# Performance work log

Hardware: AMD Instinct MI355X
Metric: run time of the kernel (lower is better)

The kernel has to match this reference:

```python
import jax, jax.numpy as jnp
import numpy as np

B, H, D = 16, 16, 128
BLOCK = 16
BLOCKS_PER_SEQ = 128
MAX_S = BLOCK * BLOCKS_PER_SEQ  # 2048
NUM_BLOCKS = B * BLOCKS_PER_SEQ  # 2048


def _rotate_half(x):
    d = x.shape[-1] // 2
    return jnp.concatenate([-x[..., d:], x[..., :d]], axis=-1)


def setup_inputs() -> dict:
    key = jax.random.key(0)
    ks = jax.random.split(key, 8)
    Q = jax.random.normal(ks[0], (B, H, D), dtype=jnp.float32)
    K = jax.random.normal(ks[1], (B, H, D), dtype=jnp.float32)
    V = jax.random.normal(ks[2], (B, H, D), dtype=jnp.float32)
    Kcache = jax.random.normal(ks[3], (NUM_BLOCKS, BLOCK, H, D), dtype=jnp.float32)
    Vcache = jax.random.normal(ks[4], (NUM_BLOCKS, BLOCK, H, D), dtype=jnp.float32)
    # RoPE tables [MAX_S, 1, D] (llama convention: half-dim freqs duplicated)
    inv_freq = 1.0 / (10000.0 ** (np.arange(0, D, 2, dtype=np.float32) / D))
    t = np.arange(MAX_S, dtype=np.float32)
    ang = np.einsum('t,f->tf', t, inv_freq)  # [MAX_S, D/2]
    emb = np.concatenate([ang, ang], axis=-1)  # [MAX_S, D]
    cos = jnp.asarray(np.cos(emb))[:, None, :]
    sin = jnp.asarray(np.sin(emb))[:, None, :]
    mask = jnp.zeros((B, MAX_S), dtype=jnp.float32)
    input_length = jnp.ones((B,), dtype=jnp.int32)
    cache_length = jax.random.randint(ks[5], (B,), 1024, MAX_S - 1).astype(jnp.int32)
    # block table: sequence b owns blocks [b*128, (b+1)*128)
    fetch_slots = (jnp.arange(B, dtype=jnp.int32)[:, None] * BLOCKS_PER_SEQ
                   + jnp.arange(BLOCKS_PER_SEQ, dtype=jnp.int32)[None, :])
    # write slot for the new token at position cache_length[b]
    blk = fetch_slots[jnp.arange(B), cache_length // BLOCK]
    save_slots = (blk * BLOCK + cache_length % BLOCK).astype(jnp.int32)
    return {"Q": Q, "K": K, "V": V, "Kcache": Kcache, "Vcache": Vcache,
            "cos": cos, "sin": sin, "mask": mask,
            "input_length": input_length, "cache_length": cache_length,
            "save_slots": save_slots, "fetch_slots": fetch_slots, "max_s": MAX_S}


def reference(Q, K, V, Kcache, Vcache, cos, sin, mask,
              input_length, cache_length, save_slots, fetch_slots, max_s):
    b, h, d = Q.shape
    block = Kcache.shape[1]
    scale = 1.0 / jnp.sqrt(jnp.asarray(d, Q.dtype))
    # RoPE on the new token at position cache_length[b]
    c = cos[cache_length]  # [B,1,D]
    s = sin[cache_length]
    Qr = Q * c + _rotate_half(Q) * s
    Kr = K * c + _rotate_half(K) * s
    # write new K/V into the paged caches at save_slots (flat slot ids)
    Kf = Kcache.reshape(-1, h, d).at[save_slots].set(Kr)
    Vf = Vcache.reshape(-1, h, d).at[save_slots].set(V)
    # gather per-sequence KV via block table -> flat slot ids [B, S]
    slot_ids = (fetch_slots[:, :, None] * block
                + jnp.arange(block, dtype=fetch_slots.dtype)).reshape(b, -1)
    Kg = Kf[slot_ids]  # [B,S,H,D]
    Vg = Vf[slot_ids]
    S = slot_ids.shape[1]
    scores = jnp.einsum('bhd,bshd->bhs', Qr, Kg) * scale + mask[:, None, :]
    valid = jnp.arange(S)[None, :] <= cache_length[:, None]  # [B,S]
    scores = jnp.where(valid[:, None, :], scores, jnp.finfo(scores.dtype).min)
    attn = jax.nn.softmax(scores, axis=-1)
    out = jnp.einsum('bhs,bshd->bhd', attn, Vg)
    return out
```

## Files before the change

kernel.cpp:

```cpp
#include <hip/hip_runtime.h>
#include <math.h>

#define PB_B      16
#define PB_H      16
#define PB_D      128
#define PB_BLOCK  16
#define PB_BPS    128
#define PB_MAXS   2048
#define PB_HD     (PB_H * PB_D)

#define NT        512
#define NSG       (NT / 32)

__global__ __launch_bounds__(NT) void paged_attn_decode(
    const float* __restrict__ Q,
    const float* __restrict__ Knew,
    const float* __restrict__ Vnew,
    const float* __restrict__ Kc,
    const float* __restrict__ Vc,
    const float* __restrict__ cosT,
    const float* __restrict__ sinT,
    const float* __restrict__ mask,
    const int*   __restrict__ cache_len,
    const int*   __restrict__ fetch_slots,
    float*       __restrict__ out)
{
    const int bh  = blockIdx.x;
    const int b   = bh >> 4;
    const int h   = bh & 15;
    const int tid = threadIdx.x;
    const int cl  = cache_len[b];
    const float scale = 0.08838834764831845f;

    __shared__ float sScore[PB_MAXS];
    __shared__ int   sSlots[PB_BPS];
    __shared__ float sQr[PB_D];
    __shared__ float sKr[PB_D];
    __shared__ float sRedM[NT / 64];
    __shared__ float sRedS[NT / 64];
    __shared__ float4 sAcc[NSG][32];

    if (tid < PB_BPS) sSlots[tid] = fetch_slots[b * PB_BPS + tid];

    if (tid < PB_D) {
        const float c = cosT[(size_t)cl * PB_D + tid];
        const float s = sinT[(size_t)cl * PB_D + tid];
        const float q = Q[(size_t)bh * PB_D + tid];
        const float k = Knew[(size_t)bh * PB_D + tid];
        const float qrot = (tid < 64) ? -Q[(size_t)bh * PB_D + tid + 64]
                                      :  Q[(size_t)bh * PB_D + tid - 64];
        const float krot = (tid < 64) ? -Knew[(size_t)bh * PB_D + tid + 64]
                                      :  Knew[(size_t)bh * PB_D + tid - 64];
        sQr[tid] = q * c + qrot * s;
        sKr[tid] = k * c + krot * s;
    }
    __syncthreads();

    const int dsub = tid & 31;
    const int ssub = tid >> 5;
    const float4 qv = ((const float4*)sQr)[dsub];
    const float* mrow = mask + (size_t)b * PB_MAXS;

    #pragma unroll 4
    for (int s = ssub; s < cl; s += NSG) {
        const int slot = sSlots[s >> 4] * PB_BLOCK + (s & 15);
        const float4 kv = ((const float4*)(Kc + (size_t)slot * PB_HD + (size_t)h * PB_D))[dsub];
        float dot = qv.x * kv.x + qv.y * kv.y + qv.z * kv.z + qv.w * kv.w;
        #pragma unroll
        for (int off = 16; off >= 1; off >>= 1) dot += __shfl_xor(dot, off);
        if (dsub == 0) sScore[s] = dot * scale + mrow[s];
    }
    if (tid < 32) {
        const float4 kv = ((const float4*)sKr)[dsub];
        float dot = qv.x * kv.x + qv.y * kv.y + qv.z * kv.z + qv.w * kv.w;
        #pragma unroll
        for (int off = 16; off >= 1; off >>= 1) dot += __shfl_xor(dot, off);
        if (dsub == 0) sScore[cl] = dot * scale + mrow[cl];
    }
    __syncthreads();

    float lm = -INFINITY;
    for (int s = tid; s <= cl; s += NT) lm = fmaxf(lm, sScore[s]);
    #pragma unroll
    for (int off = 32; off >= 1; off >>= 1) lm = fmaxf(lm, __shfl_xor(lm, off));
    if ((tid & 63) == 0) sRedM[tid >> 6] = lm;
    __syncthreads();
    float m = sRedM[0];
    #pragma unroll
    for (int w = 1; w < NT / 64; ++w) m = fmaxf(m, sRedM[w]);

    float ls = 0.0f;
    for (int s = tid; s <= cl; s += NT) {
        const float p = __expf(sScore[s] - m);
        sScore[s] = p;
        ls += p;
    }
    #pragma unroll
    for (int off = 32; off >= 1; off >>= 1) ls += __shfl_xor(ls, off);
    if ((tid & 63) == 0) sRedS[tid >> 6] = ls;
    __syncthreads();
    float sum = 0.0f;
    #pragma unroll
    for (int w = 0; w < NT / 64; ++w) sum += sRedS[w];

    float4 acc = make_float4(0.f, 0.f, 0.f, 0.f);
    #pragma unroll 4
    for (int s = ssub; s < cl; s += NSG) {
        const int slot = sSlots[s >> 4] * PB_BLOCK + (s & 15);
        const float4 vv = ((const float4*)(Vc + (size_t)slot * PB_HD + (size_t)h * PB_D))[dsub];
        const float p = sScore[s];
        acc.x += p * vv.x; acc.y += p * vv.y; acc.z += p * vv.z; acc.w += p * vv.w;
    }
    if (ssub == 0) {
        const float p = sScore[cl];
        const float4 vv = ((const float4*)(Vnew + (size_t)bh * PB_D))[dsub];
        acc.x += p * vv.x; acc.y += p * vv.y; acc.z += p * vv.z; acc.w += p * vv.w;
    }
    sAcc[ssub][dsub] = acc;
    __syncthreads();

    if (tid < 32) {
        float4 a = sAcc[0][tid];
        #pragma unroll
        for (int g = 1; g < NSG; ++g) {
            const float4 t = sAcc[g][tid];
            a.x += t.x; a.y += t.y; a.z += t.z; a.w += t.w;
        }
        const float inv = 1.0f / sum;
        a.x *= inv; a.y *= inv; a.z *= inv; a.w *= inv;
        ((float4*)(out + (size_t)bh * PB_D))[tid] = a;
    }
}

extern "C" void kernel_launch(void* const* d_in, const int* in_sizes, int n_in,
                              void* d_out, int out_size, void* d_ws, size_t ws_size,
                              hipStream_t stream) {
    const float* Q     = (const float*)d_in[0];
    const float* Knew  = (const float*)d_in[1];
    const float* Vnew  = (const float*)d_in[2];
    const float* Kc    = (const float*)d_in[3];
    const float* Vc    = (const float*)d_in[4];
    const float* cosT  = (const float*)d_in[5];
    const float* sinT  = (const float*)d_in[6];
    const float* mask  = (const float*)d_in[7];
    const int* cache_len   = (const int*)d_in[9];
    const int* fetch_slots = (const int*)d_in[11];
    float* out = (float*)d_out;

    paged_attn_decode<<<PB_B * PB_H, NT, 0, stream>>>(
        Q, Knew, Vnew, Kc, Vc, cosT, sinT, mask, cache_len, fetch_slots, out);
}
```

Before: 576.2 us.

## Split KV sequence across blocks with flash-decoding and a combine kernel

Splits each (batch, head) sequence into 8 chunks processed by separate 256-thread blocks, each producing a partial accumulator, max and sum in workspace; a second kernel merges them with log-sum-exp rescaling. The original grid of 256 blocks underfills the GPU, and the split is meant to raise parallelism and memory-level concurrency for this bandwidth-bound decode. It adds a second launch, a workspace round trip and redundant RoPE/slot loads per chunk.

New measurement: 499.6 us. 1.15x faster.

```diff
diff --git a/kernel.cpp b/kernel.cpp
--- a/kernel.cpp
+++ b/kernel.cpp
@@ -3,16 +3,19 @@
 
 #define PB_B      16
 #define PB_H      16
+#define PB_BH     (PB_B * PB_H)
 #define PB_D      128
 #define PB_BLOCK  16
 #define PB_BPS    128
 #define PB_MAXS   2048
 #define PB_HD     (PB_H * PB_D)
 
-#define NT        512
-#define NSG       (NT / 32)
-
-__global__ __launch_bounds__(NT) void paged_attn_decode(
+#define NSPLIT    8
+#define NT1       256
+#define NGRP      (NT1 / 32)
+#define MAXCHUNK  256
+
+__global__ __launch_bounds__(NT1) void pa_split(
     const float* __restrict__ Q,
     const float* __restrict__ Knew,
     const float* __restrict__ Vnew,
@@ -23,22 +26,39 @@
     const float* __restrict__ mask,
     const int*   __restrict__ cache_len,
     const int*   __restrict__ fetch_slots,
-    float*       __restrict__ out)
+    float*       __restrict__ wsAcc,
+    float*       __restrict__ wsM,
+    float*       __restrict__ wsL)
 {
-    const int bh  = blockIdx.x;
+    const int gid = blockIdx.x;
+    const int k   = gid & (NSPLIT - 1);
+    const int bh  = gid >> 3;
     const int b   = bh >> 4;
     const int h   = bh & 15;
     const int tid = threadIdx.x;
     const int cl  = cache_len[b];
+    const int n_total = cl + 1;
+    const int chunk = (n_total + NSPLIT - 1) / NSPLIT;
+    const int lo = k * chunk;
+    const int hi = min(lo + chunk, n_total);
+    const int n  = hi - lo;
     const float scale = 0.08838834764831845f;
 
-    __shared__ float sScore[PB_MAXS];
+    float* accOut = wsAcc + (size_t)gid * PB_D;
+
+    if (n <= 0) {
+        if (tid < PB_D) accOut[tid] = 0.0f;
+        if (tid == 0) { wsM[gid] = -INFINITY; wsL[gid] = 0.0f; }
+        return;
+    }
+
+    __shared__ float sScore[MAXCHUNK];
     __shared__ int   sSlots[PB_BPS];
     __shared__ float sQr[PB_D];
     __shared__ float sKr[PB_D];
-    __shared__ float sRedM[NT / 64];
-    __shared__ float sRedS[NT / 64];
-    __shared__ float4 sAcc[NSG][32];
+    __shared__ float sRed[NT1 / 64];
+    __shared__ float sRedS[NT1 / 64];
+    __shared__ float4 sAcc[NGRP][32];
 
     if (tid < PB_BPS) sSlots[tid] = fetch_slots[b * PB_BPS + tid];
 
@@ -46,90 +66,116 @@
         const float c = cosT[(size_t)cl * PB_D + tid];
         const float s = sinT[(size_t)cl * PB_D + tid];
         const float q = Q[(size_t)bh * PB_D + tid];
-        const float k = Knew[(size_t)bh * PB_D + tid];
+        const float kk = Knew[(size_t)bh * PB_D + tid];
         const float qrot = (tid < 64) ? -Q[(size_t)bh * PB_D + tid + 64]
                                       :  Q[(size_t)bh * PB_D + tid - 64];
         const float krot = (tid < 64) ? -Knew[(size_t)bh * PB_D + tid + 64]
                                       :  Knew[(size_t)bh * PB_D + tid - 64];
         sQr[tid] = q * c + qrot * s;
-        sKr[tid] = k * c + krot * s;
+        sKr[tid] = kk * c + krot * s;
     }
     __syncthreads();
 
     const int dsub = tid & 31;
-    const int ssub = tid >> 5;
+    const int grp  = tid >> 5;
     const float4 qv = ((const float4*)sQr)[dsub];
     const float* mrow = mask + (size_t)b * PB_MAXS;
 
+    const int sc_end = min(hi, cl);
     #pragma unroll 4
-    for (int s = ssub; s < cl; s += NSG) {
+    for (int s = lo + grp; s < sc_end; s += NGRP) {
         const int slot = sSlots[s >> 4] * PB_BLOCK + (s & 15);
         const float4 kv = ((const float4*)(Kc + (size_t)slot * PB_HD + (size_t)h * PB_D))[dsub];
         float dot = qv.x * kv.x + qv.y * kv.y + qv.z * kv.z + qv.w * kv.w;
         #pragma unroll
         for (int off = 16; off >= 1; off >>= 1) dot += __shfl_xor(dot, off);
-        if (dsub == 0) sScore[s] = dot * scale + mrow[s];
-    }
-    if (tid < 32) {
+        if (dsub == 0) sScore[s - lo] = dot * scale + mrow[s];
+    }
+    if (cl >= lo && cl < hi && tid < 32) {
         const float4 kv = ((const float4*)sKr)[dsub];
         float dot = qv.x * kv.x + qv.y * kv.y + qv.z * kv.z + qv.w * kv.w;
         #pragma unroll
         for (int off = 16; off >= 1; off >>= 1) dot += __shfl_xor(dot, off);
-        if (dsub == 0) sScore[cl] = dot * scale + mrow[cl];
+        if (dsub == 0) sScore[cl - lo] = dot * scale + mrow[cl];
     }
     __syncthreads();
 
     float lm = -INFINITY;
-    for (int s = tid; s <= cl; s += NT) lm = fmaxf(lm, sScore[s]);
+    for (int i = tid; i < n; i += NT1) lm = fmaxf(lm, sScore[i]);
     #pragma unroll
     for (int off = 32; off >= 1; off >>= 1) lm = fmaxf(lm, __shfl_xor(lm, off));
-    if ((tid & 63) == 0) sRedM[tid >> 6] = lm;
-    __syncthreads();
-    float m = sRedM[0];
-    #pragma unroll
-    for (int w = 1; w < NT / 64; ++w) m = fmaxf(m, sRedM[w]);
+    if ((tid & 63) == 0) sRed[tid >> 6] = lm;
+    __syncthreads();
+    float m = fmaxf(fmaxf(sRed[0], sRed[1]), fmaxf(sRed[2], sRed[3]));
 
     float ls = 0.0f;
-    for (int s = tid; s <= cl; s += NT) {
-        const float p = __expf(sScore[s] - m);
-        sScore[s] = p;
+    for (int i = tid; i < n; i += NT1) {
+        const float p = __expf(sScore[i] - m);
+        sScore[i] = p;
         ls += p;
     }
     #pragma unroll
     for (int off = 32; off >= 1; off >>= 1) ls += __shfl_xor(ls, off);
     if ((tid & 63) == 0) sRedS[tid >> 6] = ls;
     __syncthreads();
-    float sum = 0.0f;
-    #pragma unroll
-    for (int w = 0; w < NT / 64; ++w) sum += sRedS[w];
+    const float lsum = sRedS[0] + sRedS[1] + sRedS[2] + sRedS[3];
 
     float4 acc = make_float4(0.f, 0.f, 0.f, 0.f);
     #pragma unroll 4
-    for (int s = ssub; s < cl; s += NSG) {
+    for (int s = lo + grp; s < sc_end; s += NGRP) {
         const int slot = sSlots[s >> 4] * PB_BLOCK + (s & 15);
         const float4 vv = ((const float4*)(Vc + (size_t)slot * PB_HD + (size_t)h * PB_D))[dsub];
-        const float p = sScore[s];
+        const float p = sScore[s - lo];
         acc.x += p * vv.x; acc.y += p * vv.y; acc.z += p * vv.z; acc.w += p * vv.w;
     }
-    if (ssub == 0) {
-        const float p = sScore[cl];
+    if (cl >= lo && cl < hi && grp == 0) {
+        const float p = sScore[cl - lo];
         const float4 vv = ((const float4*)(Vnew + (size_t)bh * PB_D))[dsub];
         acc.x += p * vv.x; acc.y += p * vv.y; acc.z += p * vv.z; acc.w += p * vv.w;
     }
-    sAcc[ssub][dsub] = acc;
+    sAcc[grp][dsub] = acc;
     __syncthreads();
 
     if (tid < 32) {
         float4 a = sAcc[0][tid];
         #pragma unroll
-        for (int g = 1; g < NSG; ++g) {
+        for (int g = 1; g < NGRP; ++g) {
             const float4 t = sAcc[g][tid];
             a.x += t.x; a.y += t.y; a.z += t.z; a.w += t.w;
         }
-        const float inv = 1.0f / sum;
-        a.x *= inv; a.y *= inv; a.z *= inv; a.w *= inv;
-        ((float4*)(out + (size_t)bh * PB_D))[tid] = a;
-    }
+        ((float4*)accOut)[tid] = a;
+    }
+    if (tid == 0) { wsM[gid] = m; wsL[gid] = lsum; }
+}
+
+__global__ __launch_bounds__(PB_D) void pa_combine(
+    const float* __restrict__ wsAcc,
+    const float* __restrict__ wsM,
+    const float* __restrict__ wsL,
+    float*       __restrict__ out)
+{
+    const int bh = blockIdx.x;
+    const int d  = threadIdx.x;
+
+    float mv[NSPLIT];
+    float M = -INFINITY;
+    #pragma unroll
+    for (int i = 0; i < NSPLIT; ++i) {
+        mv[i] = wsM[bh * NSPLIT + i];
+        M = fmaxf(M, mv[i]);
+    }
+    float denom = 0.0f;
+    float w[NSPLIT];
+    #pragma unroll
+    for (int i = 0; i < NSPLIT; ++i) {
+        w[i] = __expf(mv[i] - M);
+        denom += w[i] * wsL[bh * NSPLIT + i];
+    }
+    float o = 0.0f;
+    #pragma unroll
+    for (int i = 0; i < NSPLIT; ++i)
+        o += w[i] * wsAcc[(size_t)(bh * NSPLIT + i) * PB_D + d];
+    out[(size_t)bh * PB_D + d] = o / denom;
 }
 
 extern "C" void kernel_launch(void* const* d_in, const int* in_sizes, int n_in,
@@ -147,6 +193,12 @@
     const int* fetch_slots = (const int*)d_in[11];
     float* out = (float*)d_out;
 
-    paged_attn_decode<<<PB_B * PB_H, NT, 0, stream>>>(
-        Q, Knew, Vnew, Kc, Vc, cosT, sinT, mask, cache_len, fetch_slots, out);
+    float* wsAcc = (float*)d_ws;
+    float* wsM   = wsAcc + (size_t)PB_BH * NSPLIT * PB_D;
+    float* wsL   = wsM + PB_BH * NSPLIT;
+
+    pa_split<<<PB_BH * NSPLIT, NT1, 0, stream>>>(
+        Q, Knew, Vnew, Kc, Vc, cosT, sinT, mask, cache_len, fetch_slots,
+        wsAcc, wsM, wsL);
+    pa_combine<<<PB_BH, PB_D, 0, stream>>>(wsAcc, wsM, wsL, out);
 }
```
